# Optimization experiments

Measured on AMD Instinct MI355X. Metric: run time of the kernel, lower is better.

Reference implementation:

```python
import jax, jax.numpy as jnp
import numpy as np

B, N, M, DIN, HID, L, NC, NH = 8, 1024, 8, 1024, 256, 2, 7, 4
DH = HID // NH
ALPHA = 0.1          # LeakyReLU slope in RGATLayer
NEG = -9e15          # masked-softmax fill value from the source


def setup_inputs() -> dict:
    key = jax.random.key(0)
    ks = jax.random.split(key, 40)
    f32 = jnp.float32
    rn = lambda k, s, sc: jax.random.normal(k, s, f32) * sc
    w = HID ** -0.5
    inp = {
        'x': rn(ks[0], (B, N, DIN), 1.0),
        'adj': jax.random.randint(ks[1], (B, N, N), 0, 2, jnp.int32),
        's_mask': jax.random.randint(ks[2], (B, N, N), 0, 2, jnp.int32),
        's_feature': rn(ks[3], (B, M, DIN), 1.0),
        's_adj': jax.random.uniform(ks[4], (B, M, N), f32),
        'speaker_id': jax.random.randint(ks[5], (B, N), 0, M, jnp.int32),
        'fc1_w': rn(ks[6], (DIN, HID), DIN ** -0.5), 'fc1_b': jnp.zeros((HID,), f32),
        'fc2_w': rn(ks[7], (DIN, HID), DIN ** -0.5), 'fc2_b': jnp.zeros((HID,), f32),
        'gat_W': rn(ks[8], (L, HID, HID), w),
        'gat_a': rn(ks[9], (L, 3 * HID), (3 * HID) ** -0.5),
        'rel_emb': rn(ks[10], (L, 2, HID), 0.1),
        'gru_wz': rn(ks[11], (L, HID, HID), 0.1), 'gru_uz': rn(ks[12], (L, HID, HID), 0.1),
        'gru_wr': rn(ks[13], (L, HID, HID), 0.1), 'gru_ur': rn(ks[14], (L, HID, HID), 0.1),
        'gru_w': rn(ks[15], (L, HID, HID), 0.1), 'gru_u': rn(ks[16], (L, HID, HID), 0.1),
        'mha_wv': rn(ks[17], (L, HID, HID), w), 'mha_bv': jnp.zeros((L, HID), f32),
        'mha_wk': rn(ks[18], (L, HID, HID), w), 'mha_bk': jnp.zeros((L, HID), f32),
        'mha_wq': rn(ks[19], (L, HID, HID), w), 'mha_bq': jnp.zeros((L, HID), f32),
        'mha_wo': rn(ks[20], (L, HID, HID), w), 'mha_bo': jnp.zeros((L, HID), f32),
        'ln_g': jnp.ones((L, HID), f32), 'ln_b': jnp.zeros((L, HID), f32),
        'out_w': rn(ks[21], (HID, NC), w), 'out_b': jnp.zeros((NC,), f32),
    }
    return inp


def _layer_norm(x, g, b):
    mu = jnp.mean(x, -1, keepdims=True)
    var = jnp.mean((x - mu) ** 2, -1, keepdims=True)
    return (x - mu) * jax.lax.rsqrt(var + 1e-5) * g + b


def reference(x, adj, s_mask, s_feature, s_adj, speaker_id,
              fc1_w, fc1_b, fc2_w, fc2_b,
              gat_W, gat_a, rel_emb,
              gru_wz, gru_uz, gru_wr, gru_ur, gru_w, gru_u,
              mha_wv, mha_bv, mha_wk, mha_bk, mha_wq, mha_bq, mha_wo, mha_bo,
              ln_g, ln_b, out_w, out_b):
    # eval mode: dropout is identity. init_way == 'global', att_agg == True.
    H = jax.nn.relu(x @ fc1_w + fc1_b)           # [B,N,HID]
    P = jax.nn.relu(s_feature @ fc2_w + fc2_b)   # [B,M,HID]
    adj_mask = adj > 0
    for l in range(L):
        P_l_1 = jnp.einsum('bmn,bmd->bnd', s_adj, P)  # s_adj^T @ P -> [B,N,HID]
        # ---- RGAT layer (decomposed: never materializes [B,N,N,3*HID]) ----
        h = H @ gat_W[l]                               # [B,N,HID]
        a1, a2, a3 = jnp.split(gat_a[l], 3)
        rel_sc = rel_emb[l] @ a3                       # (2,) per-relation score
        e = jax.nn.leaky_relu((h @ a1)[:, :, None] + (h @ a2)[:, None, :]
                              + jnp.take(rel_sc, s_mask), ALPHA)  # [B,N,N]
        att = jax.nn.softmax(jnp.where(adj_mask, e, jnp.float32(NEG)), axis=2)
        Agg = jax.nn.elu(att @ h)                      # [B,N,HID]
        # ---- Multi-head attention aggregation (replicates source's reshape) ----
        V = (H @ mha_wv[l] + mha_bv[l]).reshape(B * NH, -1, DH)
        Km = (P_l_1 @ mha_wk[l] + mha_bk[l]).reshape(B * NH, -1, DH)
        Qm = (Agg @ mha_wq[l] + mha_bq[l]).reshape(B * NH, -1, DH)
        att2 = jax.nn.softmax(jnp.einsum('bqd,bkd->bqk', Qm, Km) * DH ** -0.5, axis=-1)
        ctx = (att2 @ V).reshape(B, -1, HID)
        H_new = _layer_norm(ctx @ mha_wo[l] + mha_bo[l] + H, ln_g[l], ln_b[l])
        # ---- GRU3d speaker-state update (uses H[l], i.e. pre-update H) ----
        P_agg = jnp.einsum('bmn,bnd->bmd', s_adj, H)   # [B,M,HID]
        z = jax.nn.sigmoid(P @ gru_wz[l] + P_agg @ gru_uz[l])
        r = jax.nn.sigmoid(P @ gru_wr[l] + P_agg @ gru_ur[l])
        h_hat = jnp.tanh(P @ gru_w[l] + r * (P_agg @ gru_u[l]))
        P = (1 - z) * P + z * h_hat
        H = H_new
    # sim_loss
    ps = jnp.einsum('bmd,bkd->bmk', P, P)
    ps = ps * (1.0 - jnp.eye(M, dtype=ps.dtype))
    p_sim = jnp.mean(jnp.mean(jnp.mean(ps, -1), -1), -1)
    logits = H @ out_w + out_b
    return (logits, p_sim)
```

## Files before the change

### kernel.cpp

```cpp
#include <hip/hip_runtime.h>
#include <cmath>

#define B 8
#define N 1024
#define MSP 8
#define DIN 1024
#define HID 256
#define NLAYER 2
#define NCLS 7
#define NHEAD 4
#define DHD 64
#define G (B*NHEAD)
#define SEQ 1024
#define LALPHA 0.1f
#define NEGF (-9e15f)
#define RROWS 8

typedef unsigned short u16;
typedef unsigned int u32;
typedef __attribute__((ext_vector_type(8))) short short8;
typedef __attribute__((ext_vector_type(4))) float f32x4;

__device__ __forceinline__ u16 f2bf(float f) {
  u32 u = __float_as_uint(f);
  u += 0x7FFFu + ((u >> 16) & 1u);
  return (u16)(u >> 16);
}
__device__ __forceinline__ void stf(float* p, size_t i, float v) { p[i] = v; }
__device__ __forceinline__ void stf(u16* p, size_t i, float v) { p[i] = f2bf(v); }

__device__ __forceinline__ float wave_reduce_sum(float v) {
  #pragma unroll
  for (int o = 32; o > 0; o >>= 1) v += __shfl_xor(v, o, 64);
  return v;
}
__device__ __forceinline__ float wave_reduce_max(float v) {
  #pragma unroll
  for (int o = 32; o > 0; o >>= 1) v = fmaxf(v, __shfl_xor(v, o, 64));
  return v;
}

__device__ __forceinline__ void tcast_tile(
    const float* src, u16* dst, int ldS, int ldD, int r0, int c0, int t,
    u16* tile )
{
  #pragma unroll
  for (int i = 0; i < 4; ++i) {
    int e = i * 1024 + t * 4;
    int r = e >> 6, c = e & 63;
    float4 v = *(const float4*)&src[(size_t)(r0 + r) * ldS + c0 + c];
    u16* d = &tile[r * 72 + c];
    d[0] = f2bf(v.x); d[1] = f2bf(v.y); d[2] = f2bf(v.z); d[3] = f2bf(v.w);
  }
  __syncthreads();
  #pragma unroll
  for (int i = 0; i < 2; ++i) {
    int e = i * 2048 + t * 8;
    int r2 = e >> 6, c2 = e & 63;
    u16 v[8];
    #pragma unroll
    for (int j = 0; j < 8; ++j) v[j] = tile[(c2 + j) * 72 + r2];
    *(uint4*)&dst[(size_t)(c0 + r2) * ldD + r0 + c2] = *(const uint4*)v;
  }
}

__global__ __launch_bounds__(256) void wprep256(
    const float* g, const float* wv, const float* wk, const float* wq,
    const float* wo, const float* wz, const float* wr, const float* w,
    const float* uz, const float* ur, const float* u, u16* WT)
{
  __shared__ u16 tile[64 * 72];
  int z = blockIdx.z, idx = z >> 1, l = z & 1;
  const float* src;
  switch (idx) {
    case 0: src = g; break;  case 1: src = wv; break; case 2: src = wk; break;
    case 3: src = wq; break; case 4: src = wo; break; case 5: src = wz; break;
    case 6: src = wr; break; case 7: src = w; break;  case 8: src = uz; break;
    case 9: src = ur; break; default: src = u; break;
  }
  src += (size_t)l * 65536;
  u16* dst = WT + (size_t)z * 65536;
  tcast_tile(src, dst, 256, 256, blockIdx.x * 64, blockIdx.y * 64, threadIdx.x, tile);
}

__global__ __launch_bounds__(256) void wprepfc(
    const float* w1, const float* w2, u16* WTfc)
{
  __shared__ u16 tile[64 * 72];
  int z = blockIdx.z;
  const float* src = z ? w2 : w1;
  u16* dst = WTfc + (size_t)z * 262144;
  tcast_tile(src, dst, 256, 1024, blockIdx.x * 64, blockIdx.y * 64, threadIdx.x, tile);
}

__global__ __launch_bounds__(256) void hcast_kernel(
    const float* h, u16* ht)
{
  __shared__ u16 tile[64 * 72];
  tcast_tile(h, ht, 256, 8192, blockIdx.x * 64, blockIdx.y * 64, threadIdx.x, tile);
}

__global__ __launch_bounds__(256) void outprep(const float* ow, u16* WTout) {
  int t = threadIdx.x;
  for (int e = t; e < NCLS * 256; e += 256) {
    int n = e >> 8, k = e & 255;
    WTout[e] = f2bf(ow[k * NCLS + n]);
  }
}

__device__ __forceinline__ void stage_a(const float* p, u16* d) {
  #pragma unroll
  for (int q = 0; q < 4; ++q) {
    float4 v = *(const float4*)(p + q * 4);
    d[q * 4 + 0] = f2bf(v.x); d[q * 4 + 1] = f2bf(v.y);
    d[q * 4 + 2] = f2bf(v.z); d[q * 4 + 3] = f2bf(v.w);
  }
}
__device__ __forceinline__ void stage_a(const u16* p, u16* d) {
  *(uint4*)d = *(const uint4*)p;
  *(uint4*)(d + 8) = *(const uint4*)(p + 8);
}

template <typename TA, typename TC>
__global__ __launch_bounds__(256) void gemm_t(
    const TA* __restrict__ A, const u16* __restrict__ Wt,
    const float* __restrict__ bias, TC* __restrict__ C,
    int K, int ldA, int ldW, int Nc, int act,
    size_t sA, size_t sW, size_t sC)
{
  __shared__ u16 As[64 * 72];
  __shared__ u16 Ws[64 * 72];
  int z = blockIdx.z;
  const TA* Ab = A + (size_t)z * sA;
  const u16* Wb = Wt + (size_t)z * sW;
  TC* Cb = C + (size_t)z * sC;
  int bm = blockIdx.x * 64, bn = blockIdx.y * 64;
  int t = threadIdx.x;
  int w = t >> 6, lane = t & 63, quad = lane >> 4, l15 = lane & 15;
  int wy = w >> 1, wx = w & 1;
  int sr = t >> 2, kg = (t & 3) * 16;
  bool wok = (bn + sr) < Nc;
  f32x4 acc[2][2];
  #pragma unroll
  for (int i = 0; i < 2; ++i)
    #pragma unroll
    for (int j = 0; j < 2; ++j) acc[i][j] = (f32x4){0.f, 0.f, 0.f, 0.f};

  for (int k0 = 0; k0 < K; k0 += 64) {
    u16 av[16];
    stage_a(Ab + (size_t)(bm + sr) * ldA + k0 + kg, av);
    *(uint4*)&As[sr * 72 + kg] = *(const uint4*)av;
    *(uint4*)&As[sr * 72 + kg + 8] = *(const uint4*)(av + 8);
    if (wok) {
      *(uint4*)&Ws[sr * 72 + kg] = *(const uint4*)(Wb + (size_t)(bn + sr) * ldW + k0 + kg);
      *(uint4*)&Ws[sr * 72 + kg + 8] = *(const uint4*)(Wb + (size_t)(bn + sr) * ldW + k0 + kg + 8);
    } else {
      uint4 zz = {0, 0, 0, 0};
      *(uint4*)&Ws[sr * 72 + kg] = zz;
      *(uint4*)&Ws[sr * 72 + kg + 8] = zz;
    }
    __syncthreads();
    #pragma unroll
    for (int kh = 0; kh < 64; kh += 32) {
      short8 a0 = *(const short8*)&As[(wy * 32 + l15) * 72 + kh + quad * 8];
      short8 a1 = *(const short8*)&As[(wy * 32 + 16 + l15) * 72 + kh + quad * 8];
      short8 b0 = *(const short8*)&Ws[(wx * 32 + l15) * 72 + kh + quad * 8];
      short8 b1 = *(const short8*)&Ws[(wx * 32 + 16 + l15) * 72 + kh + quad * 8];
      acc[0][0] = __builtin_amdgcn_mfma_f32_16x16x32_bf16(a0, b0, acc[0][0], 0, 0, 0);
      acc[0][1] = __builtin_amdgcn_mfma_f32_16x16x32_bf16(a0, b1, acc[0][1], 0, 0, 0);
      acc[1][0] = __builtin_amdgcn_mfma_f32_16x16x32_bf16(a1, b0, acc[1][0], 0, 0, 0);
      acc[1][1] = __builtin_amdgcn_mfma_f32_16x16x32_bf16(a1, b1, acc[1][1], 0, 0, 0);
    }
    __syncthreads();
  }
  #pragma unroll
  for (int sa = 0; sa < 2; ++sa) {
    #pragma unroll
    for (int sb = 0; sb < 2; ++sb) {
      int col = bn + wx * 32 + sb * 16 + l15;
      if (col < Nc) {
        float bv = bias ? bias[col] : 0.f;
        #pragma unroll
        for (int r = 0; r < 4; ++r) {
          int row = bm + wy * 32 + sa * 16 + quad * 4 + r;
          float v = acc[sa][sb][r] + bv;
          if (act == 1) v = fmaxf(v, 0.f);
          else if (act == 2) v = (v > 0.f) ? v : (__expf(v) - 1.f);
          stf(Cb, (size_t)row * Nc + col, v);
        }
      }
    }
  }
}

__global__ __launch_bounds__(256) void fc2_reduce(
    const float* __restrict__ scr, const float* __restrict__ bias,
    float* __restrict__ out)
{
  int i = blockIdx.x * 256 + threadIdx.x;
  float v = scr[i] + scr[16384 + i] + scr[32768 + i] + scr[49152 + i]
          + bias[threadIdx.x];
  out[i] = fmaxf(v, 0.f);
}

__global__ __launch_bounds__(256) void gru_combine(
    const float* __restrict__ zP, const float* __restrict__ zU,
    const float* __restrict__ P, float* __restrict__ Pn)
{
  int i = blockIdx.x * 256 + threadIdx.x;
  float z = 1.f / (1.f + __expf(-(zP[i] + zU[i])));
  float r = 1.f / (1.f + __expf(-(zP[16384 + i] + zU[16384 + i])));
  float hh = tanhf(zP[32768 + i] + r * zU[32768 + i]);
  Pn[i] = (1.f - z) * P[i] + z * hh;
}

__global__ __launch_bounds__(256) void pl1_kernel(
    const float* __restrict__ s_adj, const float* __restrict__ P,
    float* __restrict__ out)
{
  int bn = blockIdx.x;
  int b = bn >> 10, n = bn & 1023, t = threadIdx.x;
  float acc = 0.f;
  #pragma unroll
  for (int m = 0; m < MSP; ++m) {
    float sa = s_adj[(size_t)(b * MSP + m) * N + n];
    acc += sa * P[(size_t)(b * MSP + m) * HID + t];
  }
  out[(size_t)bn * HID + t] = acc;
}

__global__ __launch_bounds__(256) void relsc_kernel(
    const float* __restrict__ rel_emb_l, const float* __restrict__ a3,
    float* __restrict__ rsc)
{
  __shared__ float scratch[4];
  int r = blockIdx.x, t = threadIdx.x;
  float v = rel_emb_l[r * HID + t] * a3[t];
  int wave = t >> 6, lane = t & 63;
  v = wave_reduce_sum(v);
  if (lane == 0) scratch[wave] = v;
  __syncthreads();
  if (t == 0) rsc[r] = scratch[0] + scratch[1] + scratch[2] + scratch[3];
}

__global__ __launch_bounds__(256) void f1f2_kernel(
    const float* __restrict__ h, const float* __restrict__ a12,
    float* __restrict__ f1, float* __restrict__ f2)
{
  __shared__ float s1[4], s2[4];
  int row = blockIdx.x, t = threadIdx.x;
  float hv = h[(size_t)row * HID + t];
  float v1 = hv * a12[t];
  float v2 = hv * a12[HID + t];
  int wave = t >> 6, lane = t & 63;
  v1 = wave_reduce_sum(v1);
  v2 = wave_reduce_sum(v2);
  if (lane == 0) { s1[wave] = v1; s2[wave] = v2; }
  __syncthreads();
  if (t == 0) f1[row] = s1[0] + s1[1] + s1[2] + s1[3];
  if (t == 1) f2[row] = s2[0] + s2[1] + s2[2] + s2[3];
}

__global__ __launch_bounds__(256) void rgat_scores_kernel(
    const int* __restrict__ adj, const int* __restrict__ smask,
    const float* __restrict__ f1, const float* __restrict__ f2,
    const float* __restrict__ rsc, u16* __restrict__ Pw)
{
  __shared__ float red[4][RROWS];
  int blk = blockIdx.x;
  int b = blk / (N / RROWS);
  int i0 = (blk % (N / RROWS)) * RROWS;
  int t = threadIdx.x;
  int wave = t >> 6, lane = t & 63;
  float r0 = rsc[0], r1 = rsc[1];
  int j0 = t * 4;
  float4 f2v = *(const float4*)&f2[b * N + j0];
  float ev[RROWS][4];
  #pragma unroll
  for (int r = 0; r < RROWS; ++r) {
    size_t base = ((size_t)(b * N + i0 + r)) * N + j0;
    int4 a4 = *(const int4*)&adj[base];
    int4 s4 = *(const int4*)&smask[base];
    float f1v = f1[b * N + i0 + r];
    float e;
    e = f1v + f2v.x + (s4.x ? r1 : r0); e = (e > 0.f) ? e : LALPHA * e;
    ev[r][0] = (a4.x > 0) ? e : NEGF;
    e = f1v + f2v.y + (s4.y ? r1 : r0); e = (e > 0.f) ? e : LALPHA * e;
    ev[r][1] = (a4.y > 0) ? e : NEGF;
    e = f1v + f2v.z + (s4.z ? r1 : r0); e = (e > 0.f) ? e : LALPHA * e;
    ev[r][2] = (a4.z > 0) ? e : NEGF;
    e = f1v + f2v.w + (s4.w ? r1 : r0); e = (e > 0.f) ? e : LALPHA * e;
    ev[r][3] = (a4.w > 0) ? e : NEGF;
  }
  #pragma unroll
  for (int r = 0; r < RROWS; ++r) {
    float m = fmaxf(fmaxf(ev[r][0], ev[r][1]), fmaxf(ev[r][2], ev[r][3]));
    m = wave_reduce_max(m);
    if (lane == 0) red[wave][r] = m;
  }
  __syncthreads();
  float mx[RROWS];
  #pragma unroll
  for (int r = 0; r < RROWS; ++r)
    mx[r] = fmaxf(fmaxf(red[0][r], red[1][r]), fmaxf(red[2][r], red[3][r]));
  __syncthreads();
  #pragma unroll
  for (int r = 0; r < RROWS; ++r) {
    float s = 0.f;
    #pragma unroll
    for (int c = 0; c < 4; ++c) { ev[r][c] = __expf(ev[r][c] - mx[r]); s += ev[r][c]; }
    s = wave_reduce_sum(s);
    if (lane == 0) red[wave][r] = s;
  }
  __syncthreads();
  #pragma unroll
  for (int r = 0; r < RROWS; ++r) {
    float inv = 1.f / (red[0][r] + red[1][r] + red[2][r] + red[3][r]);
    u16 o[4];
    #pragma unroll
    for (int c = 0; c < 4; ++c) o[c] = f2bf(ev[r][c] * inv);
    *(uint2*)&Pw[((size_t)(b * N + i0 + r)) * N + j0] = *(const uint2*)o;
  }
}

__global__ __launch_bounds__(256) void vtransp_kernel(
    const u16* __restrict__ Vb, u16* __restrict__ Vt)
{
  __shared__ u16 tile[64 * 72];
  int g = blockIdx.x >> 4;
  int s0 = (blockIdx.x & 15) * 64;
  int t = threadIdx.x;
  #pragma unroll
  for (int i = 0; i < 2; ++i) {
    int e = i * 256 + t;
    int sr = e >> 3, d8 = (e & 7) * 8;
    *(uint4*)&tile[sr * 72 + d8] =
        *(const uint4*)&Vb[((size_t)(g * SEQ) + s0 + sr) * DHD + d8];
  }
  __syncthreads();
  #pragma unroll
  for (int i = 0; i < 2; ++i) {
    int e = i * 256 + t;
    int dr = e >> 3, s8 = (e & 7) * 8;
    u16 v[8];
    #pragma unroll
    for (int j = 0; j < 8; ++j) v[j] = tile[(s8 + j) * 72 + dr];
    *(uint4*)&Vt[((size_t)(g * DHD) + dr) * SEQ + s0 + s8] = *(const uint4*)v;
  }
}

__global__ __launch_bounds__(256) void mha_mfma_kernel(
    const u16* __restrict__ Qb, const u16* __restrict__ Kb,
    const u16* __restrict__ Vt, float* __restrict__ ctx)
{
  __shared__ u16 Ks[64 * 72];
  __shared__ u16 Vs[64 * 72];
  __shared__ u16 Ps[4][16 * 72];
  int g = blockIdx.x >> 4;
  int q0 = (blockIdx.x & 15) * 64;
  int t = threadIdx.x;
  int w = t >> 6, lane = t & 63, quad = lane >> 4, l15 = lane & 15;
  const u16* Qrow = Qb + ((size_t)(g * SEQ) + q0 + w * 16 + l15) * DHD;
  short8 qa0 = *(const short8*)(Qrow + quad * 8);
  short8 qa1 = *(const short8*)(Qrow + 32 + quad * 8);
  const u16* Kg = Kb + (size_t)g * SEQ * DHD;
  const u16* Vg = Vt + (size_t)g * DHD * SEQ;
  int srow = t >> 3, sc8 = (t & 7) * 8;
  int srow1 = (256 + t) >> 3, sc81 = sc8;
  f32x4 O[4];
  #pragma unroll
  for (int nt = 0; nt < 4; ++nt) O[nt] = (f32x4){0.f, 0.f, 0.f, 0.f};
  float mprev[4] = {-1e30f, -1e30f, -1e30f, -1e30f};
  float lsum[4] = {0.f, 0.f, 0.f, 0.f};
  uint4 kreg[2], vreg[2];
  kreg[0] = *(const uint4*)&Kg[(size_t)srow * DHD + sc8];
  kreg[1] = *(const uint4*)&Kg[(size_t)srow1 * DHD + sc81];
  vreg[0] = *(const uint4*)&Vg[(size_t)srow * SEQ + sc8];
  vreg[1] = *(const uint4*)&Vg[(size_t)srow1 * SEQ + sc81];

  for (int kc = 0; kc < SEQ; kc += 64) {
    *(uint4*)&Ks[srow * 72 + sc8] = kreg[0];
    *(uint4*)&Ks[srow1 * 72 + sc81] = kreg[1];
    *(uint4*)&Vs[srow * 72 + sc8] = vreg[0];
    *(uint4*)&Vs[srow1 * 72 + sc81] = vreg[1];
    __syncthreads();
    if (kc + 64 < SEQ) {
      kreg[0] = *(const uint4*)&Kg[(size_t)(kc + 64 + srow) * DHD + sc8];
      kreg[1] = *(const uint4*)&Kg[(size_t)(kc + 64 + srow1) * DHD + sc81];
      vreg[0] = *(const uint4*)&Vg[(size_t)srow * SEQ + kc + 64 + sc8];
      vreg[1] = *(const uint4*)&Vg[(size_t)srow1 * SEQ + kc + 64 + sc81];
    }
    f32x4 s[4];
    #pragma unroll
    for (int st = 0; st < 4; ++st) {
      short8 b0 = *(const short8*)&Ks[(st * 16 + l15) * 72 + quad * 8];
      short8 b1 = *(const short8*)&Ks[(st * 16 + l15) * 72 + 32 + quad * 8];
      f32x4 c = (f32x4){0.f, 0.f, 0.f, 0.f};
      c = __builtin_amdgcn_mfma_f32_16x16x32_bf16(qa0, b0, c, 0, 0, 0);
      c = __builtin_amdgcn_mfma_f32_16x16x32_bf16(qa1, b1, c, 0, 0, 0);
      s[st] = c * 0.125f;
    }
    float cm[4];
    #pragma unroll
    for (int r = 0; r < 4; ++r)
      cm[r] = fmaxf(fmaxf(s[0][r], s[1][r]), fmaxf(s[2][r], s[3][r]));
    #pragma unroll
    for (int off = 1; off < 16; off <<= 1) {
      #pragma unroll
      for (int r = 0; r < 4; ++r) cm[r] = fmaxf(cm[r], __shfl_xor(cm[r], off, 64));
    }
    float mnew[4], alpha[4], rs[4];
    #pragma unroll
    for (int r = 0; r < 4; ++r) {
      mnew[r] = fmaxf(mprev[r], cm[r]);
      alpha[r] = __expf(mprev[r] - mnew[r]);
      mprev[r] = mnew[r];
      rs[r] = 0.f;
    }
    #pragma unroll
    for (int st = 0; st < 4; ++st) {
      #pragma unroll
      for (int r = 0; r < 4; ++r) {
        float p = __expf(s[st][r] - mnew[r]);
        rs[r] += p;
        Ps[w][(quad * 4 + r) * 72 + st * 16 + l15] = f2bf(p);
      }
    }
    #pragma unroll
    for (int off = 1; off < 16; off <<= 1) {
      #pragma unroll
      for (int r = 0; r < 4; ++r) rs[r] += __shfl_xor(rs[r], off, 64);
    }
    #pragma unroll
    for (int r = 0; r < 4; ++r) lsum[r] = lsum[r] * alpha[r] + rs[r];
    #pragma unroll
    for (int nt = 0; nt < 4; ++nt)
      #pragma unroll
      for (int r = 0; r < 4; ++r) O[nt][r] *= alpha[r];
    #pragma unroll
    for (int kh = 0; kh < 2; ++kh) {
      short8 pa = *(const short8*)&Ps[w][l15 * 72 + kh * 32 + quad * 8];
      #pragma unroll
      for (int nt = 0; nt < 4; ++nt) {
        short8 vb = *(const short8*)&Vs[(nt * 16 + l15) * 72 + kh * 32 + quad * 8];
        O[nt] = __builtin_amdgcn_mfma_f32_16x16x32_bf16(pa, vb, O[nt], 0, 0, 0);
      }
    }
    __syncthreads();
  }
  #pragma unroll
  for (int nt = 0; nt < 4; ++nt) {
    #pragma unroll
    for (int r = 0; r < 4; ++r) {
      size_t row = (size_t)(g * SEQ) + q0 + w * 16 + quad * 4 + r;
      ctx[row * DHD + nt * 16 + l15] = O[nt][r] / lsum[r];
    }
  }
}

__global__ __launch_bounds__(256) void ln_kernel(
    const float* __restrict__ tmp, const float* __restrict__ Hres,
    const float* __restrict__ gg, const float* __restrict__ bb,
    float* __restrict__ out)
{
  __shared__ float s1[4], s2[4];
  int row = blockIdx.x, t = threadIdx.x;
  float x = tmp[(size_t)row * HID + t] + Hres[(size_t)row * HID + t];
  float v1 = wave_reduce_sum(x);
  float v2 = wave_reduce_sum(x * x);
  int wave = t >> 6, lane = t & 63;
  if (lane == 0) { s1[wave] = v1; s2[wave] = v2; }
  __syncthreads();
  float mu = (s1[0] + s1[1] + s1[2] + s1[3]) * (1.f / HID);
  float var = (s2[0] + s2[1] + s2[2] + s2[3]) * (1.f / HID) - mu * mu;
  var = fmaxf(var, 0.f);
  float y = (x - mu) * rsqrtf(var + 1e-5f) * gg[t] + bb[t];
  out[(size_t)row * HID + t] = y;
}

__global__ __launch_bounds__(256) void pagg_part(
    const float* __restrict__ s_adj, const float* __restrict__ H,
    float* __restrict__ scr)
{
  int row = blockIdx.x;
  int sl = blockIdx.y;
  int b = row >> 3, t = threadIdx.x;
  const float* Hb = H + ((size_t)(b * N) + sl * 128) * HID + t;
  const float* sa = s_adj + (size_t)row * N + sl * 128;
  float acc = 0.f;
  #pragma unroll 4
  for (int n = 0; n < 128; ++n)
    acc += sa[n] * Hb[(size_t)n * HID];
  scr[((size_t)sl * (B * MSP) + row) * HID + t] = acc;
}
__global__ __launch_bounds__(256) void pagg_reduce(
    const float* __restrict__ scr, float* __restrict__ Pagg)
{
  int row = blockIdx.x, t = threadIdx.x;
  float s = 0.f;
  #pragma unroll
  for (int k = 0; k < 8; ++k) s += scr[((size_t)k * (B * MSP) + row) * HID + t];
  Pagg[(size_t)row * HID + t] = s;
}

__global__ __launch_bounds__(256) void psim_kernel(
    const float* __restrict__ P, float* __restrict__ out)
{
  __shared__ float scratch[4];
  int t = threadIdx.x;
  float total = 0.f;
  for (int idx = t; idx < B * MSP * MSP; idx += 256) {
    int b = idx >> 6, m = (idx >> 3) & 7, k = idx & 7;
    if (m != k) {
      const float* pm = P + (size_t)(b * MSP + m) * HID;
      const float* pk = P + (size_t)(b * MSP + k) * HID;
      float d = 0.f;
      for (int dd = 0; dd < HID; ++dd) d += pm[dd] * pk[dd];
      total += d;
    }
  }
  int wave = t >> 6, lane = t & 63;
  total = wave_reduce_sum(total);
  if (lane == 0) scratch[wave] = total;
  __syncthreads();
  if (t == 0)
    out[0] = (scratch[0] + scratch[1] + scratch[2] + scratch[3]) *
             (1.f / (B * MSP * MSP));
}

extern "C" void kernel_launch(void* const* d_in, const int* in_sizes, int n_in,
                              void* d_out, int out_size, void* d_ws, size_t ws_size,
                              hipStream_t stream) {
  const float* x      = (const float*)d_in[0];
  const int*   adj    = (const int*)d_in[1];
  const int*   smask  = (const int*)d_in[2];
  const float* s_feat = (const float*)d_in[3];
  const float* s_adj  = (const float*)d_in[4];
  const float* fc1_w  = (const float*)d_in[6];
  const float* fc1_b  = (const float*)d_in[7];
  const float* fc2_w  = (const float*)d_in[8];
  const float* fc2_b  = (const float*)d_in[9];
  const float* gat_W  = (const float*)d_in[10];
  const float* gat_a  = (const float*)d_in[11];
  const float* rel_emb= (const float*)d_in[12];
  const float* gru_wz = (const float*)d_in[13];
  const float* gru_uz = (const float*)d_in[14];
  const float* gru_wr = (const float*)d_in[15];
  const float* gru_ur = (const float*)d_in[16];
  const float* gru_w  = (const float*)d_in[17];
  const float* gru_u  = (const float*)d_in[18];
  const float* mha_wv = (const float*)d_in[19];
  const float* mha_bv = (const float*)d_in[20];
  const float* mha_wk = (const float*)d_in[21];
  const float* mha_bk = (const float*)d_in[22];
  const float* mha_wq = (const float*)d_in[23];
  const float* mha_bq = (const float*)d_in[24];
  const float* mha_wo = (const float*)d_in[25];
  const float* mha_bo = (const float*)d_in[26];
  const float* ln_g   = (const float*)d_in[27];
  const float* ln_b   = (const float*)d_in[28];
  const float* out_w  = (const float*)d_in[29];
  const float* out_b  = (const float*)d_in[30];

  float* ws = (float*)d_ws;
  const size_t BIG = (size_t)B * N * HID;
  float* H0  = ws + 0 * BIG;
  float* H1  = ws + 1 * BIG;
  float* hbf = ws + 2 * BIG;
  float* Pl1 = ws + 3 * BIG;
  float* Agg = ws + 4 * BIG;
  u16* Pw   = (u16*)(ws + 5 * BIG);
  u16* Qb16 = (u16*)(ws + 5 * BIG);
  u16* Kb16 = Qb16 + BIG;
  u16* Vb16 = (u16*)(ws + 6 * BIG);
  u16* Vt16 = Vb16 + BIG;
  u16* ht   = (u16*)(ws + 7 * BIG);
  u16* WT   = ht + 2097152;
  u16* WTfc = WT + 22 * 65536;
  u16* WTout= WTfc + 2 * 262144;
  float* scrFc = Agg;
  float* zP = hbf;
  float* zU = hbf + 3 * 16384;
  float* paggScr = hbf + 6 * 16384;
  float* smw = ws + 8 * BIG;
  float* P0   = smw;
  float* P1   = smw + 16384;
  float* Pagg = smw + 32768;
  float* f1   = smw + 49152;
  float* f2   = smw + 57344;
  float* rsc  = smw + 65536;

  dim3 blk(256);
  const size_t W64K = 65536;

  wprep256<<<dim3(4, 4, 22), blk, 0, stream>>>(
      gat_W, mha_wv, mha_wk, mha_wq, mha_wo,
      gru_wz, gru_wr, gru_w, gru_uz, gru_ur, gru_u, WT);
  wprepfc<<<dim3(16, 4, 2), blk, 0, stream>>>(fc1_w, fc2_w, WTfc);
  outprep<<<1, blk, 0, stream>>>(out_w, WTout);

  gemm_t<float, float><<<dim3(128, 4, 1), blk, 0, stream>>>(
      x, WTfc, fc1_b, H0, DIN, DIN, DIN, HID, 1, 0, 0, 0);
  gemm_t<float, float><<<dim3(1, 4, 4), blk, 0, stream>>>(
      s_feat, WTfc + 262144, nullptr, scrFc, 256, DIN, DIN, HID, 0,
      256, 256, 16384);
  fc2_reduce<<<64, blk, 0, stream>>>(scrFc, fc2_b, P0);

  float* Hc = H0; float* Hn = H1; float* Pc = P0; float* Pn = P1;
  for (int l = 0; l < NLAYER; ++l) {
    pl1_kernel<<<B * N, blk, 0, stream>>>(s_adj, Pc, Pl1);
    gemm_t<float, float><<<dim3(128, 4, 1), blk, 0, stream>>>(
        Hc, WT + (size_t)(0 + l) * W64K, nullptr, hbf, HID, HID, HID, HID, 0, 0, 0, 0);
    hcast_kernel<<<dim3(128, 4), blk, 0, stream>>>(hbf, ht);
    relsc_kernel<<<2, blk, 0, stream>>>(rel_emb + (size_t)l * 2 * HID,
                                        gat_a + (size_t)l * 3 * HID + 2 * HID, rsc);
    f1f2_kernel<<<B * N, blk, 0, stream>>>(hbf, gat_a + (size_t)l * 3 * HID, f1, f2);
    rgat_scores_kernel<<<B * (N / RROWS), blk, 0, stream>>>(adj, smask, f1, f2, rsc, Pw);
    gemm_t<u16, float><<<dim3(16, 4, 8), blk, 0, stream>>>(
        Pw, ht, nullptr, Agg, N, N, B * N, HID, 2,
        (size_t)N * N, (size_t)N, (size_t)N * HID);
    gemm_t<float, u16><<<dim3(128, 4, 1), blk, 0, stream>>>(
        Hc, WT + (size_t)(2 + l) * W64K, mha_bv + l * HID, Vb16, HID, HID, HID, HID, 0, 0, 0, 0);
    gemm_t<float, u16><<<dim3(128, 4, 1), blk, 0, stream>>>(
        Pl1, WT + (size_t)(4 + l) * W64K, mha_bk + l * HID, Kb16, HID, HID, HID, HID, 0, 0, 0, 0);
    gemm_t<float, u16><<<dim3(128, 4, 1), blk, 0, stream>>>(
        Agg, WT + (size_t)(6 + l) * W64K, mha_bq + l * HID, Qb16, HID, HID, HID, HID, 0, 0, 0, 0);
    vtransp_kernel<<<G * (SEQ / 64), blk, 0, stream>>>(Vb16, Vt16);
    mha_mfma_kernel<<<G * (SEQ / 64), blk, 0, stream>>>(Qb16, Kb16, Vt16, Agg);
    gemm_t<float, float><<<dim3(128, 4, 1), blk, 0, stream>>>(
        Agg, WT + (size_t)(8 + l) * W64K, mha_bo + l * HID, Pl1, HID, HID, HID, HID, 0, 0, 0, 0);
    ln_kernel<<<B * N, blk, 0, stream>>>(Pl1, Hc, ln_g + l * HID, ln_b + l * HID, Hn);
    pagg_part<<<dim3(B * MSP, 8), blk, 0, stream>>>(s_adj, Hc, paggScr);
    pagg_reduce<<<B * MSP, blk, 0, stream>>>(paggScr, Pagg);
    gemm_t<float, float><<<dim3(1, 4, 3), blk, 0, stream>>>(
        Pc, WT + (size_t)(10 + l) * W64K, nullptr, zP, HID, HID, HID, HID, 0,
        0, 2 * W64K, 16384);
    gemm_t<float, float><<<dim3(1, 4, 3), blk, 0, stream>>>(
        Pagg, WT + (size_t)(16 + l) * W64K, nullptr, zU, HID, HID, HID, HID, 0,
        0, 2 * W64K, 16384);
    gru_combine<<<64, blk, 0, stream>>>(zP, zU, Pc, Pn);
    float* th = Hc; Hc = Hn; Hn = th;
    float* tp = Pc; Pc = Pn; Pn = tp;
  }
  gemm_t<float, float><<<dim3(128, 1, 1), blk, 0, stream>>>(
      Hc, WTout, out_b, (float*)d_out, HID, HID, HID, NCLS, 0, 0, 0, 0);
  psim_kernel<<<1, blk, 0, stream>>>(Pc, (float*)d_out + (size_t)B * N * NCLS);
}
```

Baseline: 617.4 us.

## Batch sibling projection GEMMs via z-split, store H@W in bf16, drop MHA prefetch

The gemm_t kernel gains a second A/W/bias set selected by blockIdx.z, so the GAT projection and V projection run as one launch, Q and K as one, and the two GRU gate GEMMs as one. The GAT projection output is now written directly as bf16, and a bf16-to-bf16 transpose replaces the fp32 cast-transpose. f1f2 reads the bf16 values, which lowers precision of the attention scores. The MHA kernel loses its register prefetch of the next K/V tile and now loads it straight into LDS, which removes latency hiding but may ease register pressure.

```diff
diff --git a/kernel.cpp b/kernel.cpp
--- a/kernel.cpp
+++ b/kernel.cpp
@@ -26,6 +26,9 @@
   u += 0x7FFFu + ((u >> 16) & 1u);
   return (u16)(u >> 16);
 }
+__device__ __forceinline__ float bf2f(u16 v) {
+  return __uint_as_float(((u32)v) << 16);
+}
 __device__ __forceinline__ void stf(float* p, size_t i, float v) { p[i] = v; }
 __device__ __forceinline__ void stf(u16* p, size_t i, float v) { p[i] = f2bf(v); }
 
@@ -93,11 +96,28 @@
   tcast_tile(src, dst, 256, 1024, blockIdx.x * 64, blockIdx.y * 64, threadIdx.x, tile);
 }
 
-__global__ __launch_bounds__(256) void hcast_kernel(
-    const float* h, u16* ht)
+__global__ __launch_bounds__(256) void utransp_kernel(
+    const u16* __restrict__ src, u16* __restrict__ dst, int ldS, int ldD)
 {
   __shared__ u16 tile[64 * 72];
-  tcast_tile(h, ht, 256, 8192, blockIdx.x * 64, blockIdx.y * 64, threadIdx.x, tile);
+  int r0 = blockIdx.x * 64, c0 = blockIdx.y * 64;
+  int t = threadIdx.x;
+  #pragma unroll
+  for (int i = 0; i < 2; ++i) {
+    int e = i * 256 + t;
+    int sr = e >> 3, d8 = (e & 7) * 8;
+    *(uint4*)&tile[sr * 72 + d8] = *(const uint4*)&src[(size_t)(r0 + sr) * ldS + c0 + d8];
+  }
+  __syncthreads();
+  #pragma unroll
+  for (int i = 0; i < 2; ++i) {
+    int e = i * 256 + t;
+    int dr = e >> 3, s8 = (e & 7) * 8;
+    u16 v[8];
+    #pragma unroll
+    for (int j = 0; j < 8; ++j) v[j] = tile[(s8 + j) * 72 + dr];
+    *(uint4*)&dst[(size_t)(c0 + dr) * ldD + r0 + s8] = *(const uint4*)v;
+  }
 }
 
 __global__ __launch_bounds__(256) void outprep(const float* ow, u16* WTout) {
@@ -123,16 +143,23 @@
 
 template <typename TA, typename TC>
 __global__ __launch_bounds__(256) void gemm_t(
-    const TA* __restrict__ A, const u16* __restrict__ Wt,
-    const float* __restrict__ bias, TC* __restrict__ C,
+    const TA* __restrict__ A, const TA* __restrict__ A2, int zsplit,
+    const u16* __restrict__ Wt, const u16* __restrict__ Wt2,
+    const float* __restrict__ bias, const float* __restrict__ bias2,
+    TC* __restrict__ C,
     int K, int ldA, int ldW, int Nc, int act,
     size_t sA, size_t sW, size_t sC)
 {
   __shared__ u16 As[64 * 72];
   __shared__ u16 Ws[64 * 72];
   int z = blockIdx.z;
-  const TA* Ab = A + (size_t)z * sA;
-  const u16* Wb = Wt + (size_t)z * sW;
+  const TA* Ab; const u16* Wb; const float* bs;
+  if (z < zsplit) {
+    Ab = A + (size_t)z * sA; Wb = Wt + (size_t)z * sW; bs = bias;
+  } else {
+    int z2 = z - zsplit;
+    Ab = A2 + (size_t)z2 * sA; Wb = Wt2 + (size_t)z2 * sW; bs = bias2;
+  }
   TC* Cb = C + (size_t)z * sC;
   int bm = blockIdx.x * 64, bn = blockIdx.y * 64;
   int t = threadIdx.x;
@@ -179,7 +206,7 @@
     for (int sb = 0; sb < 2; ++sb) {
       int col = bn + wx * 32 + sb * 16 + l15;
       if (col < Nc) {
-        float bv = bias ? bias[col] : 0.f;
+        float bv = bs ? bs[col] : 0.f;
         #pragma unroll
         for (int r = 0; r < 4; ++r) {
           int row = bm + wy * 32 + sa * 16 + quad * 4 + r;
@@ -244,12 +271,12 @@
 }
 
 __global__ __launch_bounds__(256) void f1f2_kernel(
-    const float* __restrict__ h, const float* __restrict__ a12,
+    const u16* __restrict__ h, const float* __restrict__ a12,
     float* __restrict__ f1, float* __restrict__ f2)
 {
   __shared__ float s1[4], s2[4];
   int row = blockIdx.x, t = threadIdx.x;
-  float hv = h[(size_t)row * HID + t];
+  float hv = bf2f(h[(size_t)row * HID + t]);
   float v1 = hv * a12[t];
   float v2 = hv * a12[HID + t];
   int wave = t >> 6, lane = t & 63;
@@ -365,31 +392,21 @@
   short8 qa1 = *(const short8*)(Qrow + 32 + quad * 8);
   const u16* Kg = Kb + (size_t)g * SEQ * DHD;
   const u16* Vg = Vt + (size_t)g * DHD * SEQ;
-  int srow = t >> 3, sc8 = (t & 7) * 8;
-  int srow1 = (256 + t) >> 3, sc81 = sc8;
   f32x4 O[4];
   #pragma unroll
   for (int nt = 0; nt < 4; ++nt) O[nt] = (f32x4){0.f, 0.f, 0.f, 0.f};
   float mprev[4] = {-1e30f, -1e30f, -1e30f, -1e30f};
   float lsum[4] = {0.f, 0.f, 0.f, 0.f};
-  uint4 kreg[2], vreg[2];
-  kreg[0] = *(const uint4*)&Kg[(size_t)srow * DHD + sc8];
-  kreg[1] = *(const uint4*)&Kg[(size_t)srow1 * DHD + sc81];
-  vreg[0] = *(const uint4*)&Vg[(size_t)srow * SEQ + sc8];
-  vreg[1] = *(const uint4*)&Vg[(size_t)srow1 * SEQ + sc81];
 
   for (int kc = 0; kc < SEQ; kc += 64) {
-    *(uint4*)&Ks[srow * 72 + sc8] = kreg[0];
-    *(uint4*)&Ks[srow1 * 72 + sc81] = kreg[1];
-    *(uint4*)&Vs[srow * 72 + sc8] = vreg[0];
-    *(uint4*)&Vs[srow1 * 72 + sc81] = vreg[1];
+    #pragma unroll
+    for (int i = 0; i < 2; ++i) {
+      int e = i * 256 + t;
+      int row = e >> 3, c8 = (e & 7) * 8;
+      *(uint4*)&Ks[row * 72 + c8] = *(const uint4*)&Kg[(size_t)(kc + row) * DHD + c8];
+      *(uint4*)&Vs[row * 72 + c8] = *(const uint4*)&Vg[(size_t)row * SEQ + kc + c8];
+    }
     __syncthreads();
-    if (kc + 64 < SEQ) {
-      kreg[0] = *(const uint4*)&Kg[(size_t)(kc + 64 + srow) * DHD + sc8];
-      kreg[1] = *(const uint4*)&Kg[(size_t)(kc + 64 + srow1) * DHD + sc81];
-      vreg[0] = *(const uint4*)&Vg[(size_t)srow * SEQ + kc + 64 + sc8];
-      vreg[1] = *(const uint4*)&Vg[(size_t)srow1 * SEQ + kc + 64 + sc81];
-    }
     f32x4 s[4];
     #pragma unroll
     for (int st = 0; st < 4; ++st) {
@@ -566,22 +583,22 @@
   const size_t BIG = (size_t)B * N * HID;
   float* H0  = ws + 0 * BIG;
   float* H1  = ws + 1 * BIG;
-  float* hbf = ws + 2 * BIG;
+  u16* hb16 = (u16*)(ws + 2 * BIG);
+  u16* Vb16 = hb16 + BIG;
   float* Pl1 = ws + 3 * BIG;
   float* Agg = ws + 4 * BIG;
   u16* Pw   = (u16*)(ws + 5 * BIG);
   u16* Qb16 = (u16*)(ws + 5 * BIG);
   u16* Kb16 = Qb16 + BIG;
-  u16* Vb16 = (u16*)(ws + 6 * BIG);
-  u16* Vt16 = Vb16 + BIG;
+  u16* Vt16 = (u16*)(ws + 6 * BIG);
   u16* ht   = (u16*)(ws + 7 * BIG);
   u16* WT   = ht + 2097152;
   u16* WTfc = WT + 22 * 65536;
   u16* WTout= WTfc + 2 * 262144;
   float* scrFc = Agg;
-  float* zP = hbf;
-  float* zU = hbf + 3 * 16384;
-  float* paggScr = hbf + 6 * 16384;
+  float* zP = Pl1;
+  float* zU = Pl1 + 3 * 16384;
+  float* paggScr = Pl1 + 6 * 16384;
   float* smw = ws + 8 * BIG;
   float* P0   = smw;
   float* P1   = smw + 16384;
@@ -600,49 +617,46 @@
   outprep<<<1, blk, 0, stream>>>(out_w, WTout);
 
   gemm_t<float, float><<<dim3(128, 4, 1), blk, 0, stream>>>(
-      x, WTfc, fc1_b, H0, DIN, DIN, DIN, HID, 1, 0, 0, 0);
+      x, x, 99, WTfc, WTfc, fc1_b, fc1_b, H0, DIN, DIN, DIN, HID, 1, 0, 0, 0);
   gemm_t<float, float><<<dim3(1, 4, 4), blk, 0, stream>>>(
-      s_feat, WTfc + 262144, nullptr, scrFc, 256, DIN, DIN, HID, 0,
-      256, 256, 16384);
+      s_feat, s_feat, 99, WTfc + 262144, WTfc, nullptr, nullptr, scrFc,
+      256, DIN, DIN, HID, 0, 256, 256, 16384);
   fc2_reduce<<<64, blk, 0, stream>>>(scrFc, fc2_b, P0);
 
   float* Hc = H0; float* Hn = H1; float* Pc = P0; float* Pn = P1;
   for (int l = 0; l < NLAYER; ++l) {
     pl1_kernel<<<B * N, blk, 0, stream>>>(s_adj, Pc, Pl1);
-    gemm_t<float, float><<<dim3(128, 4, 1), blk, 0, stream>>>(
-        Hc, WT + (size_t)(0 + l) * W64K, nullptr, hbf, HID, HID, HID, HID, 0, 0, 0, 0);
-    hcast_kernel<<<dim3(128, 4), blk, 0, stream>>>(hbf, ht);
+    gemm_t<float, u16><<<dim3(128, 4, 2), blk, 0, stream>>>(
+        Hc, Hc, 1, WT + (size_t)(0 + l) * W64K, WT + (size_t)(2 + l) * W64K,
+        nullptr, mha_bv + l * HID, hb16, HID, HID, HID, HID, 0, 0, 0, BIG);
+    utransp_kernel<<<dim3(128, 4), blk, 0, stream>>>(hb16, ht, HID, B * N);
     relsc_kernel<<<2, blk, 0, stream>>>(rel_emb + (size_t)l * 2 * HID,
                                         gat_a + (size_t)l * 3 * HID + 2 * HID, rsc);
-    f1f2_kernel<<<B * N, blk, 0, stream>>>(hbf, gat_a + (size_t)l * 3 * HID, f1, f2);
+    f1f2_kernel<<<B * N, blk, 0, stream>>>(hb16, gat_a + (size_t)l * 3 * HID, f1, f2);
     rgat_scores_kernel<<<B * (N / RROWS), blk, 0, stream>>>(adj, smask, f1, f2, rsc, Pw);
     gemm_t<u16, float><<<dim3(16, 4, 8), blk, 0, stream>>>(
-        Pw, ht, nullptr, Agg, N, N, B * N, HID, 2,
+        Pw, Pw, 99, ht, ht, nullptr, nullptr, Agg, N, N, B * N, HID, 2,
         (size_t)N * N, (size_t)N, (size_t)N * HID);
-    gemm_t<float, u16><<<dim3(128, 4, 1), blk, 0, stream>>>(
-        Hc, WT + (size_t)(2 + l) * W64K, mha_bv + l * HID, Vb16, HID, HID, HID, HID, 0, 0, 0, 0);
-    gemm_t<float, u16><<<dim3(128, 4, 1), blk, 0, stream>>>(
-        Pl1, WT + (size_t)(4 + l) * W64K, mha_bk + l * HID, Kb16, HID, HID, HID, HID, 0, 0, 0, 0);
-    gemm_t<float, u16><<<dim3(128, 4, 1), blk, 0, stream>>>(
-        Agg, WT + (size_t)(6 + l) * W64K, mha_bq + l * HID, Qb16, HID, HID, HID, HID, 0, 0, 0, 0);
+    gemm_t<float, u16><<<dim3(128, 4, 2), blk, 0, stream>>>(
+        Agg, Pl1, 1, WT + (size_t)(6 + l) * W64K, WT + (size_t)(4 + l) * W64K,
+        mha_bq + l * HID, mha_bk + l * HID, Qb16, HID, HID, HID, HID, 0, 0, 0, BIG);
     vtransp_kernel<<<G * (SEQ / 64), blk, 0, stream>>>(Vb16, Vt16);
     mha_mfma_kernel<<<G * (SEQ / 64), blk, 0, stream>>>(Qb16, Kb16, Vt16, Agg);
     gemm_t<float, float><<<dim3(128, 4, 1), blk, 0, stream>>>(
-        Agg, WT + (size_t)(8 + l) * W64K, mha_bo + l * HID, Pl1, HID, HID, HID, HID, 0, 0, 0, 0);
+        Agg, Agg, 99, WT + (size_t)(8 + l) * W64K, WT, mha_bo + l * HID, nullptr,
+        Pl1, HID, HID, HID, HID, 0, 0, 0, 0);
     ln_kernel<<<B * N, blk, 0, stream>>>(Pl1, Hc, ln_g + l * HID, ln_b + l * HID, Hn);
     pagg_part<<<dim3(B * MSP, 8), blk, 0, stream>>>(s_adj, Hc, paggScr);
     pagg_reduce<<<B * MSP, blk, 0, stream>>>(paggScr, Pagg);
-    gemm_t<float, float><<<dim3(1, 4, 3), blk, 0, stream>>>(
-        Pc, WT + (size_t)(10 + l) * W64K, nullptr, zP, HID, HID, HID, HID, 0,
-        0, 2 * W64K, 16384);
-    gemm_t<float, float><<<dim3(1, 4, 3), blk, 0, stream>>>(
-        Pagg, WT + (size_t)(16 + l) * W64K, nullptr, zU, HID, HID, HID, HID, 0,
-        0, 2 * W64K, 16384);
+    gemm_t<float, float><<<dim3(1, 4, 6), blk, 0, stream>>>(
+        Pc, Pagg, 3, WT + (size_t)(10 + l) * W64K, WT + (size_t)(16 + l) * W64K,
+        nullptr, nullptr, zP, HID, HID, HID, HID, 0, 0, 2 * W64K, 16384);
     gru_combine<<<64, blk, 0, stream>>>(zP, zU, Pc, Pn);
     float* th = Hc; Hc = Hn; Hn = th;
     float* tp = Pc; Pc = Pn; Pn = tp;
   }
   gemm_t<float, float><<<dim3(128, 1, 1), blk, 0, stream>>>(
-      Hc, WTout, out_b, (float*)d_out, HID, HID, HID, NCLS, 0, 0, 0, 0);
+      Hc, Hc, 99, WTout, WTout, out_b, out_b, (float*)d_out,
+      HID, HID, HID, NCLS, 0, 0, 0, 0);
   psim_kernel<<<1, blk, 0, stream>>>(Pc, (float*)d_out + (size_t)B * N * NCLS);
 }
```

Measured after the change: 549.3 us. 1.12x faster.
